# Optimization experiments

Hardware: AMD Instinct MI355X
Metric: run time of the kernel (lower is better)

## Reference

```python
import math
import jax, jax.numpy as jnp
import numpy as np

B, H, S, D = 2, 16, 2048, 64


def setup_inputs() -> dict:
    key = jax.random.key(0)
    kq, kk, kv = jax.random.split(key, 3)
    query = jax.random.normal(kq, (B, H, S, D), dtype=jnp.float32)
    k = jax.random.normal(kk, (B, H, S, D), dtype=jnp.float32)
    value = jax.random.normal(kv, (B, H, S, D), dtype=jnp.float32)
    # causal mask: True = keep, broadcasts over batch and heads
    mask = jnp.tril(jnp.ones((S, S), dtype=bool))
    return {"query": query, "key": k, "value": value, "mask": mask}


def reference(query, key, value, mask):
    d_k = query.shape[-1]
    scale = 1.0 / math.sqrt(d_k)
    # (..., s1, s2) materialized scores, as in the original module
    scores = jnp.einsum("bhqd,bhkd->bhqk", query, key) * scale
    scores = jnp.where(mask, scores, -jnp.inf)
    # stable softmax = exp(x - max) / sum, same math as the torch softmax helper
    attn = jax.nn.softmax(scores, axis=-1)
    return jnp.einsum("bhqk,bhkd->bhqd", attn, value)
```

## Files before the change

### kernel.cpp

```cpp
#include <hip/hip_runtime.h>
#include <hip/hip_bf16.h>


typedef __attribute__((ext_vector_type(8))) short  s8v;
typedef __attribute__((ext_vector_type(4))) float  f4v;
typedef __attribute__((ext_vector_type(4))) unsigned int u4v;

#define SEQ 2048
#define DH  64
#define BHN 32
#define CSC 0.18033688f

#if __has_builtin(__builtin_amdgcn_exp2f)
#define EXP2(x) __builtin_amdgcn_exp2f(x)
#else
#define EXP2(x) exp2f(x)
#endif

__device__ __forceinline__ unsigned short f2bf(float x) {
  union { float f; unsigned int u; } v; v.f = x;
  return (unsigned short)((v.u + 0x7fffu + ((v.u >> 16) & 1u)) >> 16);
}
__device__ __forceinline__ float bf2f(unsigned short x) {
  union { unsigned int u; float f; } v; v.u = ((unsigned int)x) << 16;
  return v.f;
}
__device__ __forceinline__ int pack_bf2(float a, float b) {
  union { __hip_bfloat162 h; int i; } u;
  u.h = __float22bfloat162_rn(make_float2(a, b));
  return u.i;
}
__device__ __forceinline__ bool probe_is_f32(const unsigned short* p) {
  const unsigned e = (p[threadIdx.x & 63] >> 7) & 0xFFu;
  return __ballot(e >= 0x89u) != 0ULL;
}
__device__ __forceinline__ s8v cvt8(const float* p) {
  float4 a = *(const float4*)p;
  float4 b = *(const float4*)(p + 4);
  s8v r;
  r[0] = (short)f2bf(a.x); r[1] = (short)f2bf(a.y);
  r[2] = (short)f2bf(a.z); r[3] = (short)f2bf(a.w);
  r[4] = (short)f2bf(b.x); r[5] = (short)f2bf(b.y);
  r[6] = (short)f2bf(b.z); r[7] = (short)f2bf(b.w);
  return r;
}
__device__ __forceinline__ s8v cvt8s(const float* p, float s) {
  float4 a = *(const float4*)p;
  float4 b = *(const float4*)(p + 4);
  s8v r;
  r[0] = (short)f2bf(a.x * s); r[1] = (short)f2bf(a.y * s);
  r[2] = (short)f2bf(a.z * s); r[3] = (short)f2bf(a.w * s);
  r[4] = (short)f2bf(b.x * s); r[5] = (short)f2bf(b.y * s);
  r[6] = (short)f2bf(b.z * s); r[7] = (short)f2bf(b.w * s);
  return r;
}

__global__ __launch_bounds__(256) void prep_kernel(
    const void* __restrict__ Kv, const void* __restrict__ Vv,
    unsigned short* __restrict__ Kbf, unsigned short* __restrict__ Vt) {
  const int bh = blockIdx.y;
  const int s0 = blockIdx.x * 64;
  const int t  = threadIdx.x;
  if (blockIdx.z == 0) {
    const unsigned short* K16 = (const unsigned short*)Kv;
    const float*          KF  = (const float*)Kv;
    const bool isF32 = probe_is_f32(K16);
    const int sr = t >> 2, c0 = (t & 3) * 16;
    const size_t base = ((size_t)(bh * SEQ + s0 + sr)) * DH + c0;
    s8v a0, a1;
    if (!isF32) { a0 = *(const s8v*)(K16 + base); a1 = *(const s8v*)(K16 + base + 8); }
    else        { a0 = cvt8(KF + base);           a1 = cvt8(KF + base + 8); }
    *(s8v*)(Kbf + base)     = a0;
    *(s8v*)(Kbf + base + 8) = a1;
  } else {
    __shared__ __align__(16) unsigned short T[64][72];
    const unsigned short* V16 = (const unsigned short*)Vv;
    const float*          VF  = (const float*)Vv;
    const bool isF32 = probe_is_f32(V16);
    {
      const int sr = t >> 2, c0 = (t & 3) * 16;
      const size_t base = ((size_t)(bh * SEQ + s0 + sr)) * DH + c0;
      s8v a0, a1;
      if (!isF32) { a0 = *(const s8v*)(V16 + base); a1 = *(const s8v*)(V16 + base + 8); }
      else        { a0 = cvt8(VF + base);           a1 = cvt8(VF + base + 8); }
      *(s8v*)&T[sr][c0]     = a0;
      *(s8v*)&T[sr][c0 + 8] = a1;
    }
    __syncthreads();
    {
      const int d  = t & 63;
      const int hs = t >> 6;
      unsigned short* dst = Vt + (size_t)bh * SEQ * DH + (size_t)s0 * 64
                          + (size_t)d * 64 + hs * 16;
#pragma unroll
      for (int cc = 0; cc < 2; ++cc) {
        const int c  = hs * 2 + cc;
        const int kA = (c >> 2) * 32 + (c & 3) * 4;
        unsigned int wb[4];
        wb[0] = (unsigned int)T[kA + 0][d]  | ((unsigned int)T[kA + 1][d]  << 16);
        wb[1] = (unsigned int)T[kA + 2][d]  | ((unsigned int)T[kA + 3][d]  << 16);
        wb[2] = (unsigned int)T[kA + 16][d] | ((unsigned int)T[kA + 17][d] << 16);
        wb[3] = (unsigned int)T[kA + 18][d] | ((unsigned int)T[kA + 19][d] << 16);
        u4v q = { wb[0], wb[1], wb[2], wb[3] };
        *(u4v*)(dst + cc * 8) = q;
      }
    }
  }
}

__global__ __launch_bounds__(128, 2) void attn_kernel(
    const void* __restrict__ Qv, const unsigned short* __restrict__ Kbf,
    const unsigned short* __restrict__ Vt, void* __restrict__ Outv) {
  __shared__ __align__(16) unsigned short Ks[2][64][72];
  __shared__ __align__(16) unsigned short Vs[2][64][72];

  const unsigned short* Q16 = (const unsigned short*)Qv;
  const float*          QF  = (const float*)Qv;
  const bool isF32 = probe_is_f32(Q16);

  const int blk = blockIdx.x;
  const int bh  = (blk & 7) * 4 + ((blk >> 3) & 3);
  const int a   = (blk >> 5) & 7;
  const int bsl = blk >> 8;
  const int qb  = (bsl == 0) ? (7 - a) : (bsl == 1) ? (8 + a)
                : (bsl == 2) ? (23 - a) : (24 + a);

  const int tid  = threadIdx.x;
  const int w    = tid >> 6;
  const int lane = tid & 63;
  const int quad = lane >> 4;
  const int c16  = lane & 15;
  const int q0   = qb * 64 + w * 32;

  const size_t bh_off = (size_t)bh * SEQ * DH;
  const unsigned short* Kb = Kbf + bh_off;
  const unsigned short* Vb = Vt  + bh_off;

  s8v aq[2][2];
#pragma unroll
  for (int h = 0; h < 2; ++h)
#pragma unroll
    for (int kc = 0; kc < 2; ++kc) {
      const size_t idx = bh_off + (size_t)(q0 + h * 16 + c16) * DH + kc * 32 + quad * 8;
      if (isF32) aq[h][kc] = cvt8s(QF + idx, CSC);
      else {
        s8v aa = *(const s8v*)(Q16 + idx);
#pragma unroll
        for (int t = 0; t < 8; ++t)
          aa[t] = (short)f2bf(bf2f((unsigned short)aa[t]) * CSC);
        aq[h][kc] = aa;
      }
    }

  f4v o[2][4];
  float l[2] = {0.f, 0.f};
#pragma unroll
  for (int h = 0; h < 2; ++h)
#pragma unroll
    for (int i = 0; i < 4; ++i) { f4v z = {0.f, 0.f, 0.f, 0.f}; o[h][i] = z; }

  const int ntiles = qb + 1;

  const int srow = tid >> 1;
  const int scol = (tid & 1) * 32;
  const unsigned short* Kst = Kb + (size_t)srow * DH + scol;
  const unsigned short* Vst = Vb + (size_t)srow * 64 + scol;

  {
    s8v k0[4], v0[4];
#pragma unroll
    for (int j = 0; j < 4; ++j) {
      k0[j] = *(const s8v*)(Kst + j * 8);
      v0[j] = *(const s8v*)(Vst + j * 8);
    }
#pragma unroll
    for (int j = 0; j < 4; ++j) {
      *(s8v*)&Ks[0][srow][scol + j * 8] = k0[j];
      *(s8v*)&Vs[0][srow][scol + j * 8] = v0[j];
    }
  }
  __syncthreads();

  for (int kt = 0; kt < ntiles; ++kt) {
    const int cb = kt & 1, nb = cb ^ 1;
    const size_t koff = (size_t)((kt + 1 < ntiles) ? kt + 1 : 0) * (64 * DH);
    s8v nk[4], nv[4];
#pragma unroll
    for (int j = 0; j < 4; ++j) {
      nk[j] = *(const s8v*)(Kst + koff + j * 8);
      nv[j] = *(const s8v*)(Vst + koff + j * 8);
    }

    s8v kb[4][2];
#pragma unroll
    for (int nt = 0; nt < 4; ++nt) {
      kb[nt][0] = *(const s8v*)&Ks[cb][nt * 16 + c16][quad * 8];
      kb[nt][1] = *(const s8v*)&Ks[cb][nt * 16 + c16][32 + quad * 8];
    }
    s8v vb[4][2];
#pragma unroll
    for (int dt = 0; dt < 4; ++dt)
#pragma unroll
      for (int kc = 0; kc < 2; ++kc)
        vb[dt][kc] = *(const s8v*)&Vs[cb][dt * 16 + c16][(kc * 4 + quad) * 8];

    float p[2][4][4];
#pragma unroll
    for (int h = 0; h < 2; ++h)
#pragma unroll
      for (int nt = 0; nt < 4; ++nt) {
        f4v acc = {0.f, 0.f, 0.f, 0.f};
        acc = __builtin_amdgcn_mfma_f32_16x16x32_bf16(kb[nt][0], aq[h][0], acc, 0, 0, 0);
        acc = __builtin_amdgcn_mfma_f32_16x16x32_bf16(kb[nt][1], aq[h][1], acc, 0, 0, 0);
#pragma unroll
        for (int r = 0; r < 4; ++r) p[h][nt][r] = EXP2(acc[r]);
      }
    if (kt * 64 + 63 > q0) {
#pragma unroll
      for (int h = 0; h < 2; ++h) {
        const int qmk = q0 + h * 16 + c16 - kt * 64 - quad * 4;
#pragma unroll
        for (int nt = 0; nt < 4; ++nt)
#pragma unroll
          for (int r = 0; r < 4; ++r)
            if (nt * 16 + r > qmk) p[h][nt][r] = 0.f;
      }
    }
#pragma unroll
    for (int h = 0; h < 2; ++h) {
      float s = 0.f;
#pragma unroll
      for (int nt = 0; nt < 4; ++nt)
        s += (p[h][nt][0] + p[h][nt][1]) + (p[h][nt][2] + p[h][nt][3]);
      l[h] += s;
#pragma unroll
      for (int kc = 0; kc < 2; ++kc) {
        union { int d[4]; s8v v; } u;
        u.d[0] = pack_bf2(p[h][2 * kc][0],     p[h][2 * kc][1]);
        u.d[1] = pack_bf2(p[h][2 * kc][2],     p[h][2 * kc][3]);
        u.d[2] = pack_bf2(p[h][2 * kc + 1][0], p[h][2 * kc + 1][1]);
        u.d[3] = pack_bf2(p[h][2 * kc + 1][2], p[h][2 * kc + 1][3]);
#pragma unroll
        for (int dt = 0; dt < 4; ++dt)
          o[h][dt] = __builtin_amdgcn_mfma_f32_16x16x32_bf16(u.v, vb[dt][kc], o[h][dt], 0, 0, 0);
      }
    }

#pragma unroll
    for (int j = 0; j < 4; ++j) {
      *(s8v*)&Ks[nb][srow][scol + j * 8] = nk[j];
      *(s8v*)&Vs[nb][srow][scol + j * 8] = nv[j];
    }
    __syncthreads();
  }

#pragma unroll
  for (int h = 0; h < 2; ++h) {
    float lv = l[h];
    lv += __shfl_xor(lv, 16);
    lv += __shfl_xor(lv, 32);
    union { float f; int i; } lu; lu.f = lv;
    float invr[4];
#pragma unroll
    for (int rr = 0; rr < 4; ++rr) {
      union { int i; float f; } tf;
      tf.i = __builtin_amdgcn_ds_bpermute(4 * (quad * 4 + rr), lu.i);
      invr[rr] = 1.0f / tf.f;
    }
    if (isF32) {
      float* OF = (float*)Outv;
#pragma unroll
      for (int rr = 0; rr < 4; ++rr) {
        const size_t rb = bh_off + (size_t)(q0 + h * 16 + quad * 4 + rr) * DH + c16;
#pragma unroll
        for (int dt = 0; dt < 4; ++dt)
          OF[rb + dt * 16] = o[h][dt][rr] * invr[rr];
      }
    } else {
      unsigned short* O16 = (unsigned short*)Outv;
#pragma unroll
      for (int rr = 0; rr < 4; ++rr) {
        const size_t rb = bh_off + (size_t)(q0 + h * 16 + quad * 4 + rr) * DH + c16;
#pragma unroll
        for (int dt = 0; dt < 4; ++dt)
          O16[rb + dt * 16] = f2bf(o[h][dt][rr] * invr[rr]);
      }
    }
  }
}

extern "C" void kernel_launch(void* const* d_in, const int* in_sizes, int n_in,
                              void* d_out, int out_size, void* d_ws, size_t ws_size,
                              hipStream_t stream) {
  const void* Q = d_in[0];
  const void* K = d_in[1];
  const void* V = d_in[2];
  unsigned short* Kbf = (unsigned short*)d_ws;
  unsigned short* Vt  = Kbf + (size_t)BHN * SEQ * DH;

  dim3 g1(SEQ / 64, BHN, 2);
  prep_kernel<<<g1, 256, 0, stream>>>(K, V, Kbf, Vt);
  attn_kernel<<<dim3(1024), 128, 0, stream>>>(Q, Kbf, Vt, d_out);
}
```

Baseline: 140.2 us.

## Fuse K/V bf16 conversion and V transpose into attention kernel loads

Removes the separate prep kernel that converted K and V to bf16 and transposed V into a workspace. The attention kernel now loads the fp32 K and V tiles directly, converts them to bf16 in registers, and scatters V into a padded, swizzled shared-memory layout while storing the tile. This drops one launch and a full round trip of K and V through global memory. In exchange, every block re-converts the same K/V tiles and holds more fp32 data in registers for the prefetch. It also raises wave priority around the MFMA section.

```diff
diff --git a/kernel.cpp b/kernel.cpp
--- a/kernel.cpp
+++ b/kernel.cpp
@@ -4,7 +4,6 @@
 
 typedef __attribute__((ext_vector_type(8))) short  s8v;
 typedef __attribute__((ext_vector_type(4))) float  f4v;
-typedef __attribute__((ext_vector_type(4))) unsigned int u4v;
 
 #define SEQ 2048
 #define DH  64
@@ -17,6 +16,9 @@
 #define EXP2(x) exp2f(x)
 #endif
 
+#define VBUF (64 * 72 + 64)
+#define VROW(buf, d) ((buf) * VBUF + (d) * 72 + ((d) >> 4) * 16)
+
 __device__ __forceinline__ unsigned short f2bf(float x) {
   union { float f; unsigned int u; } v; v.f = x;
   return (unsigned short)((v.u + 0x7fffu + ((v.u >> 16) & 1u)) >> 16);
@@ -30,19 +32,15 @@
   u.h = __float22bfloat162_rn(make_float2(a, b));
   return u.i;
 }
+__device__ __forceinline__ s8v cvt8pk(float4 a, float4 b) {
+  union { int d[4]; s8v v; } u;
+  u.d[0] = pack_bf2(a.x, a.y); u.d[1] = pack_bf2(a.z, a.w);
+  u.d[2] = pack_bf2(b.x, b.y); u.d[3] = pack_bf2(b.z, b.w);
+  return u.v;
+}
 __device__ __forceinline__ bool probe_is_f32(const unsigned short* p) {
   const unsigned e = (p[threadIdx.x & 63] >> 7) & 0xFFu;
   return __ballot(e >= 0x89u) != 0ULL;
-}
-__device__ __forceinline__ s8v cvt8(const float* p) {
-  float4 a = *(const float4*)p;
-  float4 b = *(const float4*)(p + 4);
-  s8v r;
-  r[0] = (short)f2bf(a.x); r[1] = (short)f2bf(a.y);
-  r[2] = (short)f2bf(a.z); r[3] = (short)f2bf(a.w);
-  r[4] = (short)f2bf(b.x); r[5] = (short)f2bf(b.y);
-  r[6] = (short)f2bf(b.z); r[7] = (short)f2bf(b.w);
-  return r;
 }
 __device__ __forceinline__ s8v cvt8s(const float* p, float s) {
   float4 a = *(const float4*)p;
@@ -55,68 +53,20 @@
   return r;
 }
 
-__global__ __launch_bounds__(256) void prep_kernel(
-    const void* __restrict__ Kv, const void* __restrict__ Vv,
-    unsigned short* __restrict__ Kbf, unsigned short* __restrict__ Vt) {
-  const int bh = blockIdx.y;
-  const int s0 = blockIdx.x * 64;
-  const int t  = threadIdx.x;
-  if (blockIdx.z == 0) {
-    const unsigned short* K16 = (const unsigned short*)Kv;
-    const float*          KF  = (const float*)Kv;
-    const bool isF32 = probe_is_f32(K16);
-    const int sr = t >> 2, c0 = (t & 3) * 16;
-    const size_t base = ((size_t)(bh * SEQ + s0 + sr)) * DH + c0;
-    s8v a0, a1;
-    if (!isF32) { a0 = *(const s8v*)(K16 + base); a1 = *(const s8v*)(K16 + base + 8); }
-    else        { a0 = cvt8(KF + base);           a1 = cvt8(KF + base + 8); }
-    *(s8v*)(Kbf + base)     = a0;
-    *(s8v*)(Kbf + base + 8) = a1;
-  } else {
-    __shared__ __align__(16) unsigned short T[64][72];
-    const unsigned short* V16 = (const unsigned short*)Vv;
-    const float*          VF  = (const float*)Vv;
-    const bool isF32 = probe_is_f32(V16);
-    {
-      const int sr = t >> 2, c0 = (t & 3) * 16;
-      const size_t base = ((size_t)(bh * SEQ + s0 + sr)) * DH + c0;
-      s8v a0, a1;
-      if (!isF32) { a0 = *(const s8v*)(V16 + base); a1 = *(const s8v*)(V16 + base + 8); }
-      else        { a0 = cvt8(VF + base);           a1 = cvt8(VF + base + 8); }
-      *(s8v*)&T[sr][c0]     = a0;
-      *(s8v*)&T[sr][c0 + 8] = a1;
-    }
-    __syncthreads();
-    {
-      const int d  = t & 63;
-      const int hs = t >> 6;
-      unsigned short* dst = Vt + (size_t)bh * SEQ * DH + (size_t)s0 * 64
-                          + (size_t)d * 64 + hs * 16;
-#pragma unroll
-      for (int cc = 0; cc < 2; ++cc) {
-        const int c  = hs * 2 + cc;
-        const int kA = (c >> 2) * 32 + (c & 3) * 4;
-        unsigned int wb[4];
-        wb[0] = (unsigned int)T[kA + 0][d]  | ((unsigned int)T[kA + 1][d]  << 16);
-        wb[1] = (unsigned int)T[kA + 2][d]  | ((unsigned int)T[kA + 3][d]  << 16);
-        wb[2] = (unsigned int)T[kA + 16][d] | ((unsigned int)T[kA + 17][d] << 16);
-        wb[3] = (unsigned int)T[kA + 18][d] | ((unsigned int)T[kA + 19][d] << 16);
-        u4v q = { wb[0], wb[1], wb[2], wb[3] };
-        *(u4v*)(dst + cc * 8) = q;
-      }
-    }
-  }
-}
+union Ku { float4 f[8]; s8v h[4]; };
+union Vu { float4 f[8]; float s[32]; s8v h[4]; unsigned short us[64]; };
 
 __global__ __launch_bounds__(128, 2) void attn_kernel(
-    const void* __restrict__ Qv, const unsigned short* __restrict__ Kbf,
-    const unsigned short* __restrict__ Vt, void* __restrict__ Outv) {
+    const void* __restrict__ Qv, const void* __restrict__ Kv,
+    const void* __restrict__ Vv, void* __restrict__ Outv) {
   __shared__ __align__(16) unsigned short Ks[2][64][72];
-  __shared__ __align__(16) unsigned short Vs[2][64][72];
-
-  const unsigned short* Q16 = (const unsigned short*)Qv;
-  const float*          QF  = (const float*)Qv;
-  const bool isF32 = probe_is_f32(Q16);
+  __shared__ __align__(16) unsigned short Vs[2 * VBUF];
+
+  const unsigned short* Q16g = (const unsigned short*)Qv;
+  const float*          QFg  = (const float*)Qv;
+  const bool isF32q = probe_is_f32(Q16g);
+  const bool isF32k = probe_is_f32((const unsigned short*)Kv);
+  const bool isF32v = probe_is_f32((const unsigned short*)Vv);
 
   const int blk = blockIdx.x;
   const int bh  = (blk & 7) * 4 + ((blk >> 3) & 3);
@@ -133,8 +83,10 @@
   const int q0   = qb * 64 + w * 32;
 
   const size_t bh_off = (size_t)bh * SEQ * DH;
-  const unsigned short* Kb = Kbf + bh_off;
-  const unsigned short* Vb = Vt  + bh_off;
+  const float*          KF  = (const float*)Kv + bh_off;
+  const unsigned short* K16 = (const unsigned short*)Kv + bh_off;
+  const float*          VF  = (const float*)Vv + bh_off;
+  const unsigned short* V16 = (const unsigned short*)Vv + bh_off;
 
   s8v aq[2][2];
 #pragma unroll
@@ -142,9 +94,9 @@
 #pragma unroll
     for (int kc = 0; kc < 2; ++kc) {
       const size_t idx = bh_off + (size_t)(q0 + h * 16 + c16) * DH + kc * 32 + quad * 8;
-      if (isF32) aq[h][kc] = cvt8s(QF + idx, CSC);
+      if (isF32q) aq[h][kc] = cvt8s(QFg + idx, CSC);
       else {
-        s8v aa = *(const s8v*)(Q16 + idx);
+        s8v aa = *(const s8v*)(Q16g + idx);
 #pragma unroll
         for (int t = 0; t < 8; ++t)
           aa[t] = (short)f2bf(bf2f((unsigned short)aa[t]) * CSC);
@@ -161,35 +113,72 @@
 
   const int ntiles = qb + 1;
 
-  const int srow = tid >> 1;
-  const int scol = (tid & 1) * 32;
-  const unsigned short* Kst = Kb + (size_t)srow * DH + scol;
-  const unsigned short* Vst = Vb + (size_t)srow * 64 + scol;
+  const int kr  = tid >> 1;
+  const int khf = tid & 1;
+  const int kp  = tid >> 2;
+  const int qd  = tid & 3;
+  const int k0  = kp * 2;
+  const int slot0 = ((k0 >> 5) * 4 + ((k0 >> 2) & 3)) * 8
+                  + ((k0 >> 4) & 1) * 4 + (k0 & 3);
+
+#define LOAD_TILE(tile, ku, vu) do {                                          \
+    const size_t kOff = (size_t)((tile) * 64 + kr) * DH + khf * 32;           \
+    const size_t vOff = (size_t)((tile) * 64 + k0) * DH + qd * 16;            \
+    if (isF32k) {                                                             \
+      _Pragma("unroll")                                                       \
+      for (int j = 0; j < 8; ++j) (ku).f[j] = *(const float4*)(KF + kOff + j * 4); \
+    } else {                                                                  \
+      _Pragma("unroll")                                                       \
+      for (int j = 0; j < 4; ++j) (ku).h[j] = *(const s8v*)(K16 + kOff + j * 8); \
+    }                                                                         \
+    if (isF32v) {                                                             \
+      _Pragma("unroll")                                                       \
+      for (int j = 0; j < 4; ++j) (vu).f[j]     = *(const float4*)(VF + vOff + j * 4); \
+      _Pragma("unroll")                                                       \
+      for (int j = 0; j < 4; ++j) (vu).f[4 + j] = *(const float4*)(VF + vOff + DH + j * 4); \
+    } else {                                                                  \
+      (vu).h[0] = *(const s8v*)(V16 + vOff);                                  \
+      (vu).h[1] = *(const s8v*)(V16 + vOff + 8);                              \
+      (vu).h[2] = *(const s8v*)(V16 + vOff + DH);                             \
+      (vu).h[3] = *(const s8v*)(V16 + vOff + DH + 8);                         \
+    }                                                                         \
+  } while (0)
+
+#define STORE_TILE(nb, ku, vu) do {                                           \
+    if (isF32k) {                                                             \
+      _Pragma("unroll")                                                       \
+      for (int j = 0; j < 4; ++j)                                             \
+        *(s8v*)&Ks[nb][kr][khf * 32 + j * 8] = cvt8pk((ku).f[2 * j], (ku).f[2 * j + 1]); \
+    } else {                                                                  \
+      _Pragma("unroll")                                                       \
+      for (int j = 0; j < 4; ++j)                                             \
+        *(s8v*)&Ks[nb][kr][khf * 32 + j * 8] = (ku).h[j];                     \
+    }                                                                         \
+    if (isF32v) {                                                             \
+      _Pragma("unroll")                                                       \
+      for (int m = 0; m < 16; ++m)                                            \
+        *(unsigned int*)&Vs[VROW(nb, qd * 16 + m) + slot0] =                  \
+            (unsigned int)pack_bf2((vu).s[m], (vu).s[16 + m]);                \
+    } else {                                                                  \
+      _Pragma("unroll")                                                       \
+      for (int m = 0; m < 16; ++m)                                            \
+        *(unsigned int*)&Vs[VROW(nb, qd * 16 + m) + slot0] =                  \
+            (unsigned int)(vu).us[m] | ((unsigned int)(vu).us[16 + m] << 16); \
+    }                                                                         \
+  } while (0)
 
   {
-    s8v k0[4], v0[4];
-#pragma unroll
-    for (int j = 0; j < 4; ++j) {
-      k0[j] = *(const s8v*)(Kst + j * 8);
-      v0[j] = *(const s8v*)(Vst + j * 8);
-    }
-#pragma unroll
-    for (int j = 0; j < 4; ++j) {
-      *(s8v*)&Ks[0][srow][scol + j * 8] = k0[j];
-      *(s8v*)&Vs[0][srow][scol + j * 8] = v0[j];
-    }
+    Ku ku; Vu vu;
+    LOAD_TILE(0, ku, vu);
+    STORE_TILE(0, ku, vu);
   }
   __syncthreads();
 
   for (int kt = 0; kt < ntiles; ++kt) {
     const int cb = kt & 1, nb = cb ^ 1;
-    const size_t koff = (size_t)((kt + 1 < ntiles) ? kt + 1 : 0) * (64 * DH);
-    s8v nk[4], nv[4];
-#pragma unroll
-    for (int j = 0; j < 4; ++j) {
-      nk[j] = *(const s8v*)(Kst + koff + j * 8);
-      nv[j] = *(const s8v*)(Vst + koff + j * 8);
-    }
+    const int pt = (kt + 1 < ntiles) ? kt + 1 : 0;
+    Ku ku; Vu vu;
+    LOAD_TILE(pt, ku, vu);
 
     s8v kb[4][2];
 #pragma unroll
@@ -202,8 +191,9 @@
     for (int dt = 0; dt < 4; ++dt)
 #pragma unroll
       for (int kc = 0; kc < 2; ++kc)
-        vb[dt][kc] = *(const s8v*)&Vs[cb][dt * 16 + c16][(kc * 4 + quad) * 8];
-
+        vb[dt][kc] = *(const s8v*)&Vs[VROW(cb, dt * 16 + c16) + (kc * 4 + quad) * 8];
+
+    __builtin_amdgcn_s_setprio(1);
     float p[2][4][4];
 #pragma unroll
     for (int h = 0; h < 2; ++h)
@@ -245,12 +235,9 @@
           o[h][dt] = __builtin_amdgcn_mfma_f32_16x16x32_bf16(u.v, vb[dt][kc], o[h][dt], 0, 0, 0);
       }
     }
-
-#pragma unroll
-    for (int j = 0; j < 4; ++j) {
-      *(s8v*)&Ks[nb][srow][scol + j * 8] = nk[j];
-      *(s8v*)&Vs[nb][srow][scol + j * 8] = nv[j];
-    }
+    __builtin_amdgcn_s_setprio(0);
+
+    STORE_TILE(nb, ku, vu);
     __syncthreads();
   }
 
@@ -267,7 +254,7 @@
       tf.i = __builtin_amdgcn_ds_bpermute(4 * (quad * 4 + rr), lu.i);
       invr[rr] = 1.0f / tf.f;
     }
-    if (isF32) {
+    if (isF32q) {
       float* OF = (float*)Outv;
 #pragma unroll
       for (int rr = 0; rr < 4; ++rr) {
@@ -295,10 +282,6 @@
   const void* Q = d_in[0];
   const void* K = d_in[1];
   const void* V = d_in[2];
-  unsigned short* Kbf = (unsigned short*)d_ws;
-  unsigned short* Vt  = Kbf + (size_t)BHN * SEQ * DH;
-
-  dim3 g1(SEQ / 64, BHN, 2);
-  prep_kernel<<<g1, 256, 0, stream>>>(K, V, Kbf, Vt);
-  attn_kernel<<<dim3(1024), 128, 0, stream>>>(Q, Kbf, Vt, d_out);
-}
+  (void)d_ws; (void)ws_size; (void)in_sizes; (void)n_in; (void)out_size;
+  attn_kernel<<<dim3(1024), 128, 0, stream>>>(Q, K, V, d_out);
+}
```

Measured after the change: 156.0 us. +11.3%, slower.

## Drop LDS staging; single-wave blocks load K/V fragments directly from global

Applied to the files above, without the earlier changes.

Attention blocks shrink from two waves (64 queries) to one wave (32 queries), so the grid doubles and the query-block ordering is remapped. The double-buffered LDS staging of K and V tiles and the per-tile __syncthreads are removed. Each lane now loads its MFMA fragments straight from global memory, relying on the prep kernel's layout and on L2/L1 for reuse. This gets rid of LDS traffic and barriers but loses the cross-wave sharing of K/V and the software prefetch, which exposes global load latency inside the loop.

```diff
diff --git a/kernel.cpp b/kernel.cpp
--- a/kernel.cpp
+++ b/kernel.cpp
@@ -108,33 +108,25 @@
   }
 }
 
-__global__ __launch_bounds__(128, 2) void attn_kernel(
+__global__ __launch_bounds__(64, 3) void attn_kernel(
     const void* __restrict__ Qv, const unsigned short* __restrict__ Kbf,
     const unsigned short* __restrict__ Vt, void* __restrict__ Outv) {
-  __shared__ __align__(16) unsigned short Ks[2][64][72];
-  __shared__ __align__(16) unsigned short Vs[2][64][72];
-
   const unsigned short* Q16 = (const unsigned short*)Qv;
   const float*          QF  = (const float*)Qv;
   const bool isF32 = probe_is_f32(Q16);
 
   const int blk = blockIdx.x;
   const int bh  = (blk & 7) * 4 + ((blk >> 3) & 3);
-  const int a   = (blk >> 5) & 7;
-  const int bsl = blk >> 8;
-  const int qb  = (bsl == 0) ? (7 - a) : (bsl == 1) ? (8 + a)
-                : (bsl == 2) ? (23 - a) : (24 + a);
-
-  const int tid  = threadIdx.x;
-  const int w    = tid >> 6;
-  const int lane = tid & 63;
+  const int i   = blk >> 5;
+  const int qb  = (i & 1) ? ((i - 1) >> 1) : (63 - (i >> 1));
+
+  const int lane = threadIdx.x & 63;
   const int quad = lane >> 4;
   const int c16  = lane & 15;
-  const int q0   = qb * 64 + w * 32;
+  const int q0   = qb * 32;
+  const int ntiles = (qb >> 1) + 1;
 
   const size_t bh_off = (size_t)bh * SEQ * DH;
-  const unsigned short* Kb = Kbf + bh_off;
-  const unsigned short* Vb = Vt  + bh_off;
 
   s8v aq[2][2];
 #pragma unroll
@@ -157,52 +149,27 @@
 #pragma unroll
   for (int h = 0; h < 2; ++h)
 #pragma unroll
-    for (int i = 0; i < 4; ++i) { f4v z = {0.f, 0.f, 0.f, 0.f}; o[h][i] = z; }
-
-  const int ntiles = qb + 1;
-
-  const int srow = tid >> 1;
-  const int scol = (tid & 1) * 32;
-  const unsigned short* Kst = Kb + (size_t)srow * DH + scol;
-  const unsigned short* Vst = Vb + (size_t)srow * 64 + scol;
-
-  {
-    s8v k0[4], v0[4];
-#pragma unroll
-    for (int j = 0; j < 4; ++j) {
-      k0[j] = *(const s8v*)(Kst + j * 8);
-      v0[j] = *(const s8v*)(Vst + j * 8);
-    }
-#pragma unroll
-    for (int j = 0; j < 4; ++j) {
-      *(s8v*)&Ks[0][srow][scol + j * 8] = k0[j];
-      *(s8v*)&Vs[0][srow][scol + j * 8] = v0[j];
-    }
-  }
-  __syncthreads();
+    for (int i2 = 0; i2 < 4; ++i2) { f4v z = {0.f, 0.f, 0.f, 0.f}; o[h][i2] = z; }
+
+  const unsigned short* kp = Kbf + bh_off + (size_t)c16 * DH + quad * 8;
+  const unsigned short* vp = Vt  + bh_off + (size_t)c16 * 64 + quad * 8;
 
   for (int kt = 0; kt < ntiles; ++kt) {
-    const int cb = kt & 1, nb = cb ^ 1;
-    const size_t koff = (size_t)((kt + 1 < ntiles) ? kt + 1 : 0) * (64 * DH);
-    s8v nk[4], nv[4];
-#pragma unroll
-    for (int j = 0; j < 4; ++j) {
-      nk[j] = *(const s8v*)(Kst + koff + j * 8);
-      nv[j] = *(const s8v*)(Vst + koff + j * 8);
-    }
+    const unsigned short* kpt = kp + (size_t)kt * 4096;
+    const unsigned short* vpt = vp + (size_t)kt * 4096;
 
     s8v kb[4][2];
 #pragma unroll
-    for (int nt = 0; nt < 4; ++nt) {
-      kb[nt][0] = *(const s8v*)&Ks[cb][nt * 16 + c16][quad * 8];
-      kb[nt][1] = *(const s8v*)&Ks[cb][nt * 16 + c16][32 + quad * 8];
-    }
+    for (int nt = 0; nt < 4; ++nt)
+#pragma unroll
+      for (int kc = 0; kc < 2; ++kc)
+        kb[nt][kc] = *(const s8v*)(kpt + nt * 1024 + kc * 32);
     s8v vb[4][2];
 #pragma unroll
     for (int dt = 0; dt < 4; ++dt)
 #pragma unroll
       for (int kc = 0; kc < 2; ++kc)
-        vb[dt][kc] = *(const s8v*)&Vs[cb][dt * 16 + c16][(kc * 4 + quad) * 8];
+        vb[dt][kc] = *(const s8v*)(vpt + dt * 1024 + kc * 32);
 
     float p[2][4][4];
 #pragma unroll
@@ -245,13 +212,6 @@
           o[h][dt] = __builtin_amdgcn_mfma_f32_16x16x32_bf16(u.v, vb[dt][kc], o[h][dt], 0, 0, 0);
       }
     }
-
-#pragma unroll
-    for (int j = 0; j < 4; ++j) {
-      *(s8v*)&Ks[nb][srow][scol + j * 8] = nk[j];
-      *(s8v*)&Vs[nb][srow][scol + j * 8] = nv[j];
-    }
-    __syncthreads();
   }
 
 #pragma unroll
@@ -300,5 +260,5 @@
 
   dim3 g1(SEQ / 64, BHN, 2);
   prep_kernel<<<g1, 256, 0, stream>>>(K, V, Kbf, Vt);
-  attn_kernel<<<dim3(1024), 128, 0, stream>>>(Q, Kbf, Vt, d_out);
-}
+  attn_kernel<<<dim3(2048), 64, 0, stream>>>(Q, Kbf, Vt, d_out);
+}
```

After: 196.2 us. 40.0% more time.

## Stage K/V tiles via direct global-to-LDS loads with XOR-swizzled layout

Applied to the files above, without the earlier changes.

The prep kernel now writes K and transposed V in an XOR-swizzled 128-byte row layout, so the attention kernel can copy each tile straight into LDS with global_load_lds and no register round trip. Wave 0 loads K and wave 1 loads V for the next tile, and fragment reads use matching swizzled offsets to avoid bank conflicts without padding. s_setprio raises priority around the MFMA section. This removes the VGPR staging and the explicit LDS stores, but correctness depends on the async loads landing before the barrier and on the swizzle matching on both sides.

```diff
diff --git a/kernel.cpp b/kernel.cpp
--- a/kernel.cpp
+++ b/kernel.cpp
@@ -53,6 +53,11 @@
   r[4] = (short)f2bf(b.x * s); r[5] = (short)f2bf(b.y * s);
   r[6] = (short)f2bf(b.z * s); r[7] = (short)f2bf(b.w * s);
   return r;
+}
+__device__ __forceinline__ void gld16(const void* g, void* l) {
+  __builtin_amdgcn_global_load_lds(
+      (const __attribute__((address_space(1))) void*)g,
+      (__attribute__((address_space(3))) void*)l, 16, 0, 0);
 }
 
 __global__ __launch_bounds__(256) void prep_kernel(
@@ -65,13 +70,16 @@
     const unsigned short* K16 = (const unsigned short*)Kv;
     const float*          KF  = (const float*)Kv;
     const bool isF32 = probe_is_f32(K16);
-    const int sr = t >> 2, c0 = (t & 3) * 16;
-    const size_t base = ((size_t)(bh * SEQ + s0 + sr)) * DH + c0;
+    const int sr  = t >> 2;
+    const int cb0 = (t & 3) * 32;
+    const int xs  = (sr & 7) << 4;
+    const size_t src = ((size_t)(bh * SEQ + s0 + sr)) * DH + (t & 3) * 16;
     s8v a0, a1;
-    if (!isF32) { a0 = *(const s8v*)(K16 + base); a1 = *(const s8v*)(K16 + base + 8); }
-    else        { a0 = cvt8(KF + base);           a1 = cvt8(KF + base + 8); }
-    *(s8v*)(Kbf + base)     = a0;
-    *(s8v*)(Kbf + base + 8) = a1;
+    if (!isF32) { a0 = *(const s8v*)(K16 + src); a1 = *(const s8v*)(K16 + src + 8); }
+    else        { a0 = cvt8(KF + src);           a1 = cvt8(KF + src + 8); }
+    char* rowp = (char*)Kbf + ((size_t)(bh * SEQ + s0 + sr)) * 128;
+    *(s8v*)(rowp + (cb0 ^ xs))        = a0;
+    *(s8v*)(rowp + ((cb0 + 16) ^ xs)) = a1;
   } else {
     __shared__ __align__(16) unsigned short T[64][72];
     const unsigned short* V16 = (const unsigned short*)Vv;
@@ -90,8 +98,9 @@
     {
       const int d  = t & 63;
       const int hs = t >> 6;
-      unsigned short* dst = Vt + (size_t)bh * SEQ * DH + (size_t)s0 * 64
-                          + (size_t)d * 64 + hs * 16;
+      const int xs = (d & 7) << 4;
+      char* rowp = (char*)Vt + (size_t)bh * SEQ * 128 + (size_t)s0 * 128
+                 + (size_t)d * 128;
 #pragma unroll
       for (int cc = 0; cc < 2; ++cc) {
         const int c  = hs * 2 + cc;
@@ -102,7 +111,7 @@
         wb[2] = (unsigned int)T[kA + 16][d] | ((unsigned int)T[kA + 17][d] << 16);
         wb[3] = (unsigned int)T[kA + 18][d] | ((unsigned int)T[kA + 19][d] << 16);
         u4v q = { wb[0], wb[1], wb[2], wb[3] };
-        *(u4v*)(dst + cc * 8) = q;
+        *(u4v*)(rowp + ((c * 16) ^ xs)) = q;
       }
     }
   }
@@ -111,8 +120,7 @@
 __global__ __launch_bounds__(128, 2) void attn_kernel(
     const void* __restrict__ Qv, const unsigned short* __restrict__ Kbf,
     const unsigned short* __restrict__ Vt, void* __restrict__ Outv) {
-  __shared__ __align__(16) unsigned short Ks[2][64][72];
-  __shared__ __align__(16) unsigned short Vs[2][64][72];
+  __shared__ __align__(16) char Lds[2][16384];
 
   const unsigned short* Q16 = (const unsigned short*)Qv;
   const float*          QF  = (const float*)Qv;
@@ -133,8 +141,6 @@
   const int q0   = qb * 64 + w * 32;
 
   const size_t bh_off = (size_t)bh * SEQ * DH;
-  const unsigned short* Kb = Kbf + bh_off;
-  const unsigned short* Vb = Vt  + bh_off;
 
   s8v aq[2][2];
 #pragma unroll
@@ -161,49 +167,47 @@
 
   const int ntiles = qb + 1;
 
-  const int srow = tid >> 1;
-  const int scol = (tid & 1) * 32;
-  const unsigned short* Kst = Kb + (size_t)srow * DH + scol;
-  const unsigned short* Vst = Vb + (size_t)srow * 64 + scol;
-
-  {
-    s8v k0[4], v0[4];
-#pragma unroll
-    for (int j = 0; j < 4; ++j) {
-      k0[j] = *(const s8v*)(Kst + j * 8);
-      v0[j] = *(const s8v*)(Vst + j * 8);
-    }
-#pragma unroll
-    for (int j = 0; j < 4; ++j) {
-      *(s8v*)&Ks[0][srow][scol + j * 8] = k0[j];
-      *(s8v*)&Vs[0][srow][scol + j * 8] = v0[j];
-    }
-  }
+  const int xorl = (c16 & 7) << 4;
+  const int fc0  = (quad * 16) ^ xorl;
+  const int fc1  = (64 + quad * 16) ^ xorl;
+  const int frow = c16 * 128;
+
+  const unsigned short* Kg = Kbf + bh_off + (size_t)lane * 8;
+  const unsigned short* Vg = Vt  + bh_off + (size_t)lane * 8;
+
+  auto stage = [&](int tile, int buf) {
+    if (w == 0) {
+      const unsigned short* g = Kg + (size_t)tile * 4096;
+      char* lp = &Lds[buf][0];
+#pragma unroll
+      for (int j = 0; j < 8; ++j) gld16(g + j * 512, lp + j * 1024);
+    } else {
+      const unsigned short* g = Vg + (size_t)tile * 4096;
+      char* lp = &Lds[buf][8192];
+#pragma unroll
+      for (int j = 0; j < 8; ++j) gld16(g + j * 512, lp + j * 1024);
+    }
+  };
+
+  stage(0, 0);
   __syncthreads();
 
   for (int kt = 0; kt < ntiles; ++kt) {
     const int cb = kt & 1, nb = cb ^ 1;
-    const size_t koff = (size_t)((kt + 1 < ntiles) ? kt + 1 : 0) * (64 * DH);
-    s8v nk[4], nv[4];
-#pragma unroll
-    for (int j = 0; j < 4; ++j) {
-      nk[j] = *(const s8v*)(Kst + koff + j * 8);
-      nv[j] = *(const s8v*)(Vst + koff + j * 8);
-    }
-
-    s8v kb[4][2];
+    if (kt + 1 < ntiles) stage(kt + 1, nb);
+
+    const char* Kl = &Lds[cb][0];
+    const char* Vl = &Lds[cb][8192];
+    s8v kb[4][2], vb[4][2];
 #pragma unroll
     for (int nt = 0; nt < 4; ++nt) {
-      kb[nt][0] = *(const s8v*)&Ks[cb][nt * 16 + c16][quad * 8];
-      kb[nt][1] = *(const s8v*)&Ks[cb][nt * 16 + c16][32 + quad * 8];
-    }
-    s8v vb[4][2];
-#pragma unroll
-    for (int dt = 0; dt < 4; ++dt)
-#pragma unroll
-      for (int kc = 0; kc < 2; ++kc)
-        vb[dt][kc] = *(const s8v*)&Vs[cb][dt * 16 + c16][(kc * 4 + quad) * 8];
-
+      kb[nt][0] = *(const s8v*)(Kl + frow + nt * 2048 + fc0);
+      kb[nt][1] = *(const s8v*)(Kl + frow + nt * 2048 + fc1);
+      vb[nt][0] = *(const s8v*)(Vl + frow + nt * 2048 + fc0);
+      vb[nt][1] = *(const s8v*)(Vl + frow + nt * 2048 + fc1);
+    }
+
+    __builtin_amdgcn_s_setprio(1);
     float p[2][4][4];
 #pragma unroll
     for (int h = 0; h < 2; ++h)
@@ -245,12 +249,8 @@
           o[h][dt] = __builtin_amdgcn_mfma_f32_16x16x32_bf16(u.v, vb[dt][kc], o[h][dt], 0, 0, 0);
       }
     }
-
-#pragma unroll
-    for (int j = 0; j < 4; ++j) {
-      *(s8v*)&Ks[nb][srow][scol + j * 8] = nk[j];
-      *(s8v*)&Vs[nb][srow][scol + j * 8] = nv[j];
-    }
+    __builtin_amdgcn_s_setprio(0);
+
     __syncthreads();
   }
 
```

New measurement: 138.5 us. Within noise of the previous version (-1.2%).
